# Kernel tuning notes

Hardware: AMD Instinct MI355X
Metric: run time of the kernel (lower is better)

## Reference

```python
import jax, jax.numpy as jnp
import numpy as np

B, N, E = 4, 2048, 512
H = 8
HD = E // H
HIDDEN = 3 * E  # split_ratio=3
EPS = 1e-5


def _layernorm(x, g, b):
    mu = jnp.mean(x, axis=-1, keepdims=True)
    var = jnp.var(x, axis=-1, keepdims=True)
    return (x - mu) * jax.lax.rsqrt(var + EPS) * g + b


def setup_inputs() -> dict:
    key = jax.random.key(0)
    ks = jax.random.split(key, 7)
    s = 0.02
    return {
        "x": jax.random.normal(ks[0], (B, N, E), jnp.float32),
        "qkv_w": jax.random.normal(ks[1], (E, 3 * E), jnp.float32) * s,
        "qkv_b": jax.random.normal(ks[2], (3 * E,), jnp.float32) * s,
        "fc1_w": jax.random.normal(ks[3], (E, HIDDEN), jnp.float32) * s,
        "fc1_b": jax.random.normal(ks[4], (HIDDEN,), jnp.float32) * s,
        "fc2_w": jax.random.normal(ks[5], (HIDDEN, E), jnp.float32) * s,
        "fc2_b": jax.random.normal(ks[6], (E,), jnp.float32) * s,
        "ln_att_g": jnp.ones((E,), jnp.float32),
        "ln_att_b": jnp.zeros((E,), jnp.float32),
        "ln_ffn_g": jnp.ones((E,), jnp.float32),
        "ln_ffn_b": jnp.zeros((E,), jnp.float32),
    }


def reference(x, qkv_w, qkv_b, fc1_w, fc1_b, fc2_w, fc2_b,
              ln_att_g, ln_att_b, ln_ffn_g, ln_ffn_b):
    # --- attention sub-block (pre-norm) ---
    h = x
    xn = _layernorm(x, ln_att_g, ln_att_b)
    qkv = xn @ qkv_w + qkv_b                     # [B,N,3E]
    qkv = qkv.reshape(B, N, H, 3 * HD).transpose(0, 2, 1, 3)  # [B,H,N,3*HD]
    q, k, v = jnp.split(qkv, 3, axis=-1)         # each [B,H,N,HD]
    scale = HD ** -0.5
    scores = jnp.einsum("bhnd,bhmd->bhnm", q, k) * scale
    attn = jax.nn.softmax(scores, axis=-1)
    out = jnp.einsum("bhnm,bhmd->bhnd", attn, v)
    out = out.transpose(0, 2, 1, 3).reshape(B, N, E)
    x = out + h
    # --- FFN sub-block (pre-norm) ---
    h = x
    xn = _layernorm(x, ln_ffn_g, ln_ffn_b)
    y = jax.nn.gelu(xn @ fc1_w + fc1_b, approximate=False)
    y = y @ fc2_w + fc2_b
    return y + h
```

## Files before the change

### kernel.cpp

```cpp
#include <hip/hip_runtime.h>
#include <hip/hip_bf16.h>
#include <math.h>

typedef unsigned short ushort_t;
typedef unsigned int   uint32;

typedef __bf16 bf16x8 __attribute__((ext_vector_type(8)));
typedef float  floatx4 __attribute__((ext_vector_type(4)));

__device__ __forceinline__ float lo16(uint32 u) { return __uint_as_float(u << 16); }
__device__ __forceinline__ float hi16(uint32 u) { return __uint_as_float(u & 0xFFFF0000u); }
__device__ __forceinline__ float b2f(ushort_t u) { return __uint_as_float(((uint32)u) << 16); }
__device__ __forceinline__ ushort_t f2b(float f) {
    uint32 x = __float_as_uint(f);
    x += 0x7FFFu + ((x >> 16) & 1u);
    return (ushort_t)(x >> 16);
}
__device__ __forceinline__ bool bf_mode(const uint32* sniff) {
    return *sniff == 0x3F803F80u;
}
__device__ __forceinline__ float rd(const void* p, size_t i, bool bf) {
    return bf ? b2f(((const ushort_t*)p)[i]) : ((const float*)p)[i];
}
__device__ __forceinline__ float4 rd4(const void* p, size_t i, bool bf) {
    if (bf) {
        uint2 u = *(const uint2*)((const ushort_t*)p + i);
        float4 r; r.x = lo16(u.x); r.y = hi16(u.x); r.z = lo16(u.y); r.w = hi16(u.y);
        return r;
    }
    return *(const float4*)((const float*)p + i);
}
__device__ __forceinline__ float fexp2(float x) {
#if __has_builtin(__builtin_amdgcn_exp2f)
    return __builtin_amdgcn_exp2f(x);
#else
    return exp2f(x);
#endif
}
__device__ __forceinline__ void async_cp16(const ushort_t* g, ushort_t* l) {
    __builtin_amdgcn_global_load_lds(
        (const __attribute__((address_space(1))) void*)g,
        (__attribute__((address_space(3))) void*)l, 16, 0, 0);
}
__device__ __forceinline__ float gelu_f(float x) {
    float u = 0.79788456f * x * (1.0f + 0.044715f * x * x);
    u = fminf(u, 40.0f);
    float e = exp2f(u * 2.88539008f);
    return x * e * __builtin_amdgcn_rcpf(e + 1.0f);
}

__global__ __launch_bounds__(256)
void sentinel(float* out, float val, int n)
{
    int i = blockIdx.x * 256 + threadIdx.x;
    if (i < n) out[i] = val;
}

__global__ __launch_bounds__(256)
void conv_transpose3(const void* __restrict__ w0, const void* __restrict__ w1,
                     const void* __restrict__ w2, ushort_t* __restrict__ t0,
                     ushort_t* __restrict__ t1, ushort_t* __restrict__ t2,
                     const uint32* __restrict__ sniff)
{
    __shared__ ushort_t s[32][33];
    bool bf = bf_mode(sniff);
    int z = blockIdx.y;
    const void* W  = (z == 0) ? w0 : (z == 1) ? w1 : w2;
    ushort_t* Wt   = (z == 0) ? t0 : (z == 1) ? t1 : t2;
    int K = (z == 2) ? 1536 : 512;
    int N = (z == 2) ? 512 : 1536;
    int nb = N >> 5;
    int bx = blockIdx.x;
    int n0 = (bx % nb) * 32, k0 = (bx / nb) * 32;

    int tx = threadIdx.x & 31, ty = threadIdx.x >> 5;
#pragma unroll
    for (int i = 0; i < 4; i++) {
        int r = ty + i * 8;
        size_t idx = (size_t)(k0 + r) * N + (n0 + tx);
        s[r][tx] = f2b(rd(W, idx, bf));
    }
    __syncthreads();
#pragma unroll
    for (int i = 0; i < 4; i++) {
        int r = ty + i * 8;
        Wt[(size_t)(n0 + r) * K + (k0 + tx)] = s[tx][r];
    }
}

__global__ __launch_bounds__(256)
void v_transpose(const ushort_t* __restrict__ hbuf, ushort_t* __restrict__ vt)
{
    __shared__ ushort_t s[32][33];
    int tx = threadIdx.x & 31, ty = threadIdx.x >> 5;
    int n0 = blockIdx.x * 32, d0 = blockIdx.y * 32;
    int bh = blockIdx.z;
    int b = bh >> 3, h = bh & 7;
#pragma unroll
    for (int i = 0; i < 4; i++) {
        int r = ty + i * 8;
        s[r][tx] = hbuf[(size_t)(b * 2048 + n0 + r) * 1536 + h * 192 + 128 + d0 + tx];
    }
    __syncthreads();
#pragma unroll
    for (int i = 0; i < 4; i++) {
        int r = ty + i * 8;
        vt[((size_t)bh * 64 + d0 + r) * 2048 + n0 + tx] = s[tx][r];
    }
}

template <int XMODE>
__global__ __launch_bounds__(256)
void ln_any(const void* __restrict__ x, const void* __restrict__ g,
            const void* __restrict__ bta, ushort_t* __restrict__ out,
            const uint32* __restrict__ sniff)
{
    bool bf = bf_mode(sniff);
    int wid = threadIdx.x >> 6, lane = threadIdx.x & 63;
    int row = blockIdx.x * 4 + wid;
    size_t base = (size_t)row * 512 + (size_t)lane * 8;

    float4 v0, v1;
    if (XMODE == 2) { v0 = rd4(x, base, false); v1 = rd4(x, base + 4, false); }
    else            { v0 = rd4(x, base, bf);    v1 = rd4(x, base + 4, bf); }
    float v[8] = {v0.x, v0.y, v0.z, v0.w, v1.x, v1.y, v1.z, v1.w};

    float s = 0.f, ss = 0.f;
#pragma unroll
    for (int i = 0; i < 8; i++) { s += v[i]; ss += v[i] * v[i]; }
#pragma unroll
    for (int off = 32; off; off >>= 1) {
        s  += __shfl_xor(s, off);
        ss += __shfl_xor(ss, off);
    }
    float mu  = s * (1.0f / 512.0f);
    float var = ss * (1.0f / 512.0f) - mu * mu;
    float rs  = rsqrtf(var + 1e-5f);

    float4 g0 = rd4(g, lane * 8, bf), g1 = rd4(g, lane * 8 + 4, bf);
    float4 b0 = rd4(bta, lane * 8, bf), b1 = rd4(bta, lane * 8 + 4, bf);
    float gv[8] = {g0.x, g0.y, g0.z, g0.w, g1.x, g1.y, g1.z, g1.w};
    float bv[8] = {b0.x, b0.y, b0.z, b0.w, b1.x, b1.y, b1.z, b1.w};

    ushort_t o[8];
#pragma unroll
    for (int i = 0; i < 8; i++) o[i] = f2b((v[i] - mu) * rs * gv[i] + bv[i]);
    uint4 ov;
    ov.x = (uint32)o[0] | ((uint32)o[1] << 16);
    ov.y = (uint32)o[2] | ((uint32)o[3] << 16);
    ov.z = (uint32)o[4] | ((uint32)o[5] << 16);
    ov.w = (uint32)o[6] | ((uint32)o[7] << 16);
    *(uint4*)(out + base) = ov;
}

template <int TJ, int MODE>
__global__ __launch_bounds__(256)
void gemm_bt(const ushort_t* __restrict__ A, const ushort_t* __restrict__ Bt,
             const void* __restrict__ bias, void* C,
             const float* resid, int M, int N, int K,
             const uint32* __restrict__ sniff)
{
    constexpr int BN = 32 * TJ;
    __shared__ ushort_t As[128][32];
    __shared__ ushort_t Bs[BN][32];

    bool bf = bf_mode(sniff);
    int tid = threadIdx.x;
    int wid = tid >> 6, lane = tid & 63;
    int m0 = blockIdx.y * 128, n0 = blockIdx.x * BN;
    int wm = (wid >> 1) * 64, wn = (wid & 1) * (16 * TJ);
    int lm = lane & 15, kq = lane >> 4;

    floatx4 acc[4][TJ];
#pragma unroll
    for (int i = 0; i < 4; i++)
#pragma unroll
        for (int j = 0; j < TJ; j++) acc[i][j] = (floatx4)(0.f);

    for (int k0 = 0; k0 < K; k0 += 32) {
        __syncthreads();
#pragma unroll
        for (int i = 0; i < 2; i++) {
            int lin = i * 256 + tid;
            int r = lin >> 2, c8 = (lin & 3) * 8;
            async_cp16(&A[(size_t)(m0 + r) * K + k0 + c8], &As[r][c8]);
        }
#pragma unroll
        for (int i = 0; i < BN / 64; i++) {
            int lin = i * 256 + tid;
            int r = lin >> 2, c8 = (lin & 3) * 8;
            async_cp16(&Bt[(size_t)(n0 + r) * K + k0 + c8], &Bs[r][c8]);
        }
        __syncthreads();

        bf16x8 af[4], bfr[TJ];
#pragma unroll
        for (int ti = 0; ti < 4; ti++)
            af[ti] = *(const bf16x8*)&As[wm + ti * 16 + lm][kq * 8];
#pragma unroll
        for (int tj = 0; tj < TJ; tj++)
            bfr[tj] = *(const bf16x8*)&Bs[wn + tj * 16 + lm][kq * 8];
#pragma unroll
        for (int ti = 0; ti < 4; ti++)
#pragma unroll
            for (int tj = 0; tj < TJ; tj++)
                acc[ti][tj] = __builtin_amdgcn_mfma_f32_16x16x32_bf16(
                    af[ti], bfr[tj], acc[ti][tj], 0, 0, 0);
    }

    float bv[TJ];
#pragma unroll
    for (int tj = 0; tj < TJ; tj++) bv[tj] = rd(bias, n0 + wn + tj * 16 + lm, bf);
#pragma unroll
    for (int ti = 0; ti < 4; ti++) {
        int grow_base = m0 + wm + ti * 16 + kq * 4;
#pragma unroll
        for (int tj = 0; tj < TJ; tj++) {
            int gcol = n0 + wn + tj * 16 + lm;
#pragma unroll
            for (int r = 0; r < 4; r++) {
                int grow = grow_base + r;
                float v = acc[ti][tj][r] + bv[tj];
                if (MODE == 1) v = gelu_f(v);
                if (MODE == 2) {
                    float rv = resid[(size_t)grow * N + gcol];
                    ((float*)C)[(size_t)grow * N + gcol] = v + rv;
                } else {
                    ((ushort_t*)C)[(size_t)grow * N + gcol] = f2b(v);
                }
            }
        }
    }
}

template <int MODE>
__global__ __launch_bounds__(256)
void vgemm(const ushort_t* __restrict__ A, const void* __restrict__ W,
           const void* __restrict__ bias, void* C,
           const float* resid, int M, int N, int K,
             const uint32* __restrict__ sniff)
{
    __shared__ float Ast[32][33];
    __shared__ float Bs[32][36];

    bool bf = bf_mode(sniff);
    int t  = threadIdx.x;
    int tx = t & 15, ty = t >> 4;
    int m0 = blockIdx.y * 32, n0 = blockIdx.x * 32;
    int sr = t >> 3, sc4 = (t & 7) * 4;

    float a00 = 0.f, a01 = 0.f, a10 = 0.f, a11 = 0.f;

    for (int k0 = 0; k0 < K; k0 += 32) {
        __syncthreads();
        {
            uint2 u = *(const uint2*)&A[(size_t)(m0 + sr) * K + k0 + sc4];
            Ast[sc4 + 0][sr] = lo16(u.x);
            Ast[sc4 + 1][sr] = hi16(u.x);
            Ast[sc4 + 2][sr] = lo16(u.y);
            Ast[sc4 + 3][sr] = hi16(u.y);
        }
        {
            float4 w = rd4(W, (size_t)(k0 + sr) * N + n0 + sc4, bf);
            *(float4*)&Bs[sr][sc4] = w;
        }
        __syncthreads();

#pragma unroll
        for (int kk = 0; kk < 32; kk++) {
            float av0 = Ast[kk][ty], av1 = Ast[kk][ty + 16];
            float bv0 = Bs[kk][tx],  bv1 = Bs[kk][tx + 16];
            a00 += av0 * bv0; a01 += av0 * bv1;
            a10 += av1 * bv0; a11 += av1 * bv1;
        }
    }

    float accs[4] = {a00, a01, a10, a11};
#pragma unroll
    for (int q = 0; q < 4; q++) {
        int row = m0 + ty + (q >> 1) * 16;
        int col = n0 + tx + (q & 1) * 16;
        float v = accs[q] + rd(bias, col, bf);
        if (MODE == 1) v = gelu_f(v);
        if (MODE == 2) {
            float rv = resid[(size_t)row * N + col];
            ((float*)C)[(size_t)row * N + col] = v + rv;
        } else {
            ((ushort_t*)C)[(size_t)row * N + col] = f2b(v);
        }
    }
}

__global__ __launch_bounds__(256)
void attn_flash(const ushort_t* __restrict__ qkv, const ushort_t* __restrict__ vt,
                const void* __restrict__ x, float* __restrict__ out,
                const uint32* __restrict__ sniff)
{
    __shared__ ushort_t Kl[64][72];
    __shared__ ushort_t Vl[64][72];
    __shared__ ushort_t Pl[128][68];

    bool bf = bf_mode(sniff);
    int tid = threadIdx.x;
    int wid = tid >> 6, lane = tid & 63;
    int lm = lane & 15, quad = lane >> 4;
    int qt = blockIdx.x & 15;
    int h  = (blockIdx.x >> 4) & 7;
    int b  = blockIdx.x >> 7;
    int bh = b * 8 + h;
    int q0 = qt * 128;

    const float SC = 0.18033688011f;

    bf16x8 qf[2][2];
#pragma unroll
    for (int g = 0; g < 2; g++) {
        const ushort_t* qp = qkv +
            ((size_t)(b * 2048 + q0 + wid * 32 + g * 16 + lm) * 1536 + h * 192);
        union { bf16x8 v; ushort_t u[8]; } qa0, qa1;
        qa0.v = *(const bf16x8*)(qp + quad * 8);
        qa1.v = *(const bf16x8*)(qp + 32 + quad * 8);
#pragma unroll
        for (int i = 0; i < 8; i++) {
            qa0.u[i] = f2b(b2f(qa0.u[i]) * SC);
            qa1.u[i] = f2b(b2f(qa1.u[i]) * SC);
        }
        qf[g][0] = qa0.v; qf[g][1] = qa1.v;
    }

    floatx4 oacc[2][4];
#pragma unroll
    for (int g = 0; g < 2; g++)
#pragma unroll
        for (int dt = 0; dt < 4; dt++) oacc[g][dt] = (floatx4)(0.f);
    float lsum[2][4];
#pragma unroll
    for (int g = 0; g < 2; g++)
#pragma unroll
        for (int r = 0; r < 4; r++) lsum[g][r] = 0.f;

    int srow = tid >> 3;
    int sc8  = (tid & 7) * 8;

    const ushort_t* kb0 = qkv + ((size_t)(b * 2048 + srow)      * 1536 + h * 192 + 64 + sc8);
    const ushort_t* kb1 = qkv + ((size_t)(b * 2048 + 32 + srow) * 1536 + h * 192 + 64 + sc8);
    const ushort_t* vb0 = vt + ((size_t)bh * 64 + srow)      * 2048 + sc8;
    const ushort_t* vb1 = vt + ((size_t)bh * 64 + 32 + srow) * 2048 + sc8;

    uint4 kr0 = *(const uint4*)(kb0);
    uint4 kr1 = *(const uint4*)(kb1);
    uint4 vr0 = *(const uint4*)(vb0);
    uint4 vr1 = *(const uint4*)(vb1);

    for (int kv = 0; kv < 2048; kv += 64) {
        __syncthreads();
        *(uint4*)&Kl[srow][sc8]      = kr0;
        *(uint4*)&Kl[32 + srow][sc8] = kr1;
        *(uint4*)&Vl[srow][sc8]      = vr0;
        *(uint4*)&Vl[32 + srow][sc8] = vr1;
        __syncthreads();

        {
            int nkv = (kv + 64) & 2047;
            kr0 = *(const uint4*)(kb0 + (size_t)nkv * 1536);
            kr1 = *(const uint4*)(kb1 + (size_t)nkv * 1536);
            vr0 = *(const uint4*)(vb0 + nkv);
            vr1 = *(const uint4*)(vb1 + nkv);
        }

        floatx4 sacc[2][4];
#pragma unroll
        for (int g = 0; g < 2; g++)
#pragma unroll
            for (int t = 0; t < 4; t++) sacc[g][t] = (floatx4)(0.f);
        __builtin_amdgcn_s_setprio(1);
#pragma unroll
        for (int t = 0; t < 4; t++) {
            bf16x8 kf0 = *(const bf16x8*)&Kl[t * 16 + lm][quad * 8];
            bf16x8 kf1 = *(const bf16x8*)&Kl[t * 16 + lm][32 + quad * 8];
#pragma unroll
            for (int g = 0; g < 2; g++) {
                sacc[g][t] = __builtin_amdgcn_mfma_f32_16x16x32_bf16(qf[g][0], kf0, sacc[g][t], 0, 0, 0);
                sacc[g][t] = __builtin_amdgcn_mfma_f32_16x16x32_bf16(qf[g][1], kf1, sacc[g][t], 0, 0, 0);
            }
        }
        __builtin_amdgcn_s_setprio(0);

#pragma unroll
        for (int g = 0; g < 2; g++)
#pragma unroll
            for (int t = 0; t < 4; t++) {
#pragma unroll
                for (int r = 0; r < 4; r++) {
                    float pv = fexp2(sacc[g][t][r]);
                    lsum[g][r] += pv;
                    Pl[wid * 32 + g * 16 + quad * 4 + r][t * 16 + lm] =
                        (ushort_t)(__float_as_uint(pv) >> 16);
                }
            }

        bf16x8 pf[2][2];
#pragma unroll
        for (int g = 0; g < 2; g++) {
            pf[g][0] = *(const bf16x8*)&Pl[wid * 32 + g * 16 + lm][quad * 8];
            pf[g][1] = *(const bf16x8*)&Pl[wid * 32 + g * 16 + lm][32 + quad * 8];
        }
        __builtin_amdgcn_s_setprio(1);
#pragma unroll
        for (int dt = 0; dt < 4; dt++) {
            bf16x8 vf0 = *(const bf16x8*)&Vl[dt * 16 + lm][quad * 8];
            bf16x8 vf1 = *(const bf16x8*)&Vl[dt * 16 + lm][32 + quad * 8];
#pragma unroll
            for (int g = 0; g < 2; g++) {
                oacc[g][dt] = __builtin_amdgcn_mfma_f32_16x16x32_bf16(pf[g][0], vf0, oacc[g][dt], 0, 0, 0);
                oacc[g][dt] = __builtin_amdgcn_mfma_f32_16x16x32_bf16(pf[g][1], vf1, oacc[g][dt], 0, 0, 0);
            }
        }
        __builtin_amdgcn_s_setprio(0);
    }

    float rinv[2][4];
#pragma unroll
    for (int g = 0; g < 2; g++)
#pragma unroll
        for (int r = 0; r < 4; r++) {
            float rs = lsum[g][r];
            rs += __shfl_xor(rs, 1);
            rs += __shfl_xor(rs, 2);
            rs += __shfl_xor(rs, 4);
            rs += __shfl_xor(rs, 8);
            rinv[g][r] = __builtin_amdgcn_rcpf(rs);
        }

#pragma unroll
    for (int g = 0; g < 2; g++)
#pragma unroll
        for (int dt = 0; dt < 4; dt++) {
#pragma unroll
            for (int r = 0; r < 4; r++) {
                int row = q0 + wid * 32 + g * 16 + quad * 4 + r;
                int col = h * 64 + dt * 16 + lm;
                size_t idx = (size_t)(b * 2048 + row) * 512 + col;
                out[idx] = oacc[g][dt][r] * rinv[g][r] + rd(x, idx, bf);
            }
        }
}

extern "C" void kernel_launch(void* const* d_in, const int* in_sizes, int n_in,
                              void* d_out, int out_size, void* d_ws, size_t ws_size,
                              hipStream_t stream)
{
    static const int expect[11] = {4194304, 786432, 1536, 786432, 1536, 786432,
                                   512, 512, 512, 512, 512};
    bool ok = (n_in == 11);
    if (ok) for (int i = 0; i < 11; i++) if (in_sizes[i] != expect[i]) { ok = false; break; }
    int nblk = (out_size + 255) / 256;
    if (!ok) {
        sentinel<<<nblk, 256, 0, stream>>>((float*)d_out, 1.0e6f, out_size);
        return;
    }
    if (ws_size < (size_t)33554432) {
        sentinel<<<nblk, 256, 0, stream>>>((float*)d_out, 2.0e6f, out_size);
        return;
    }

    const void* x     = d_in[0];
    const void* qkv_w = d_in[1];
    const void* qkv_b = d_in[2];
    const void* fc1_w = d_in[3];
    const void* fc1_b = d_in[4];
    const void* fc2_w = d_in[5];
    const void* fc2_b = d_in[6];
    const void* ln1g  = d_in[7];
    const void* ln1b  = d_in[8];
    const void* ln2g  = d_in[9];
    const void* ln2b  = d_in[10];
    const uint32* sniff = (const uint32*)d_in[7];

    char* ws = (char*)d_ws;
    ushort_t* xn   = (ushort_t*)(ws);
    ushort_t* hbuf = (ushort_t*)(ws + 8388608);
    float*    x2   = (float*)d_out;
    ushort_t* vt   = xn;

    bool mfma_path = (ws_size >= (size_t)38273024);

    if (mfma_path) {
        ushort_t* wtq = (ushort_t*)(ws + 33554432);
        ushort_t* wt1 = (ushort_t*)(ws + 35127296);
        ushort_t* wt2 = (ushort_t*)(ws + 36700160);

        conv_transpose3<<<dim3(768, 3), 256, 0, stream>>>(qkv_w, fc1_w, fc2_w,
                                                          wtq, wt1, wt2, sniff);
        ln_any<0><<<2048, 256, 0, stream>>>(x, ln1g, ln1b, xn, sniff);
        gemm_bt<4, 0><<<dim3(12, 64), 256, 0, stream>>>(xn, wtq, qkv_b, hbuf, nullptr,
                                                        8192, 1536, 512, sniff);
        v_transpose<<<dim3(64, 2, 32), 256, 0, stream>>>(hbuf, vt);
        attn_flash<<<512, 256, 0, stream>>>(hbuf, vt, x, x2, sniff);
        ln_any<2><<<2048, 256, 0, stream>>>(x2, ln2g, ln2b, xn, sniff);
        gemm_bt<4, 1><<<dim3(12, 64), 256, 0, stream>>>(xn, wt1, fc1_b, hbuf, nullptr,
                                                        8192, 1536, 512, sniff);
        gemm_bt<2, 2><<<dim3(8, 64), 256, 0, stream>>>(hbuf, wt2, fc2_b, d_out, x2,
                                                       8192, 512, 1536, sniff);
    } else {
        ln_any<0><<<2048, 256, 0, stream>>>(x, ln1g, ln1b, xn, sniff);
        vgemm<0><<<dim3(48, 256), 256, 0, stream>>>(xn, qkv_w, qkv_b, hbuf, nullptr,
                                                    8192, 1536, 512, sniff);
        v_transpose<<<dim3(64, 2, 32), 256, 0, stream>>>(hbuf, vt);
        attn_flash<<<512, 256, 0, stream>>>(hbuf, vt, x, x2, sniff);
        ln_any<2><<<2048, 256, 0, stream>>>(x2, ln2g, ln2b, xn, sniff);
        vgemm<1><<<dim3(48, 256), 256, 0, stream>>>(xn, fc1_w, fc1_b, hbuf, nullptr,
                                                    8192, 1536, 512, sniff);
        vgemm<2><<<dim3(16, 256), 256, 0, stream>>>(hbuf, fc2_w, fc2_b, d_out, x2,
                                                    8192, 512, 1536, sniff);
    }
}
```

Measured before the change: 265.8 us.

## Double-buffer flash attention K/V, keep P in registers via bpermute, swizzle blocks

The attention kernel now double-buffers K/V tiles in LDS, which removes one barrier per iteration. It computes S transposed (K as the A operand) so each lane holds one query column, and it packs the probabilities into bf16 and redistributes them with ds_bpermute, removing the LDS round trip through the Pl buffer. Row sums are reduced across quads instead of within 16 lanes. Block IDs in both the GEMM and attention kernels are remapped in groups of eight to improve cache locality, at the cost of extra permute instructions and more LDS for the second buffer.

```diff
diff --git a/kernel.cpp b/kernel.cpp
--- a/kernel.cpp
+++ b/kernel.cpp
@@ -35,6 +35,13 @@
     return __builtin_amdgcn_exp2f(x);
 #else
     return exp2f(x);
+#endif
+}
+__device__ __forceinline__ uint32 pack_bf16(float e0, float e1) {
+#if __has_builtin(__builtin_amdgcn_perm)
+    return __builtin_amdgcn_perm(__float_as_uint(e1), __float_as_uint(e0), 0x07060302u);
+#else
+    return (__float_as_uint(e0) >> 16) | (__float_as_uint(e1) & 0xFFFF0000u);
 #endif
 }
 __device__ __forceinline__ void async_cp16(const ushort_t* g, ushort_t* l) {
@@ -167,7 +174,13 @@
     bool bf = bf_mode(sniff);
     int tid = threadIdx.x;
     int wid = tid >> 6, lane = tid & 63;
-    int m0 = blockIdx.y * 128, n0 = blockIdx.x * BN;
+
+    int nwgx = gridDim.x;
+    int wg   = blockIdx.y * nwgx + blockIdx.x;
+    int cpx  = (nwgx * gridDim.y) >> 3;
+    int swz  = (wg & 7) * cpx + (wg >> 3);
+    int m0 = (swz / nwgx) * 128, n0 = (swz % nwgx) * BN;
+
     int wm = (wid >> 1) * 64, wn = (wid & 1) * (16 * TJ);
     int lm = lane & 15, kq = lane >> 4;
 
@@ -296,17 +309,19 @@
                 const void* __restrict__ x, float* __restrict__ out,
                 const uint32* __restrict__ sniff)
 {
-    __shared__ ushort_t Kl[64][72];
-    __shared__ ushort_t Vl[64][72];
-    __shared__ ushort_t Pl[128][68];
+    __shared__ ushort_t Kl[2][64][72];
+    __shared__ ushort_t Vl[2][64][72];
 
     bool bf = bf_mode(sniff);
     int tid = threadIdx.x;
     int wid = tid >> 6, lane = tid & 63;
     int lm = lane & 15, quad = lane >> 4;
-    int qt = blockIdx.x & 15;
-    int h  = (blockIdx.x >> 4) & 7;
-    int b  = blockIdx.x >> 7;
+
+    int bid = blockIdx.x;
+    int swz = (bid & 7) * 64 + (bid >> 3);
+    int qt = swz & 15;
+    int h  = (swz >> 4) & 7;
+    int b  = swz >> 7;
     int bh = b * 8 + h;
     int q0 = qt * 128;
 
@@ -333,11 +348,7 @@
     for (int g = 0; g < 2; g++)
 #pragma unroll
         for (int dt = 0; dt < 4; dt++) oacc[g][dt] = (floatx4)(0.f);
-    float lsum[2][4];
-#pragma unroll
-    for (int g = 0; g < 2; g++)
-#pragma unroll
-        for (int r = 0; r < 4; r++) lsum[g][r] = 0.f;
+    float lsum[2] = {0.f, 0.f};
 
     int srow = tid >> 3;
     int sc8  = (tid & 7) * 8;
@@ -351,17 +362,28 @@
     uint4 kr1 = *(const uint4*)(kb1);
     uint4 vr0 = *(const uint4*)(vb0);
     uint4 vr1 = *(const uint4*)(vb1);
-
+    *(uint4*)&Kl[0][srow][sc8]      = kr0;
+    *(uint4*)&Kl[0][32 + srow][sc8] = kr1;
+    *(uint4*)&Vl[0][srow][sc8]      = vr0;
+    *(uint4*)&Vl[0][32 + srow][sc8] = vr1;
+    kr0 = *(const uint4*)(kb0 + (size_t)64 * 1536);
+    kr1 = *(const uint4*)(kb1 + (size_t)64 * 1536);
+    vr0 = *(const uint4*)(vb0 + 64);
+    vr1 = *(const uint4*)(vb1 + 64);
+    __syncthreads();
+
+    int addr0 = (lm + ((quad & 1) << 5)) << 2;
+    int addr1 = addr0 + 64;
+    bool hiq  = (quad >> 1) != 0;
+
+    int p = 0;
     for (int kv = 0; kv < 2048; kv += 64) {
-        __syncthreads();
-        *(uint4*)&Kl[srow][sc8]      = kr0;
-        *(uint4*)&Kl[32 + srow][sc8] = kr1;
-        *(uint4*)&Vl[srow][sc8]      = vr0;
-        *(uint4*)&Vl[32 + srow][sc8] = vr1;
-        __syncthreads();
-
-        {
-            int nkv = (kv + 64) & 2047;
+        if (kv < 2048 - 64) {
+            *(uint4*)&Kl[p ^ 1][srow][sc8]      = kr0;
+            *(uint4*)&Kl[p ^ 1][32 + srow][sc8] = kr1;
+            *(uint4*)&Vl[p ^ 1][srow][sc8]      = vr0;
+            *(uint4*)&Vl[p ^ 1][32 + srow][sc8] = vr1;
+            int nkv = (kv + 128) & 2047;
             kr0 = *(const uint4*)(kb0 + (size_t)nkv * 1536);
             kr1 = *(const uint4*)(kb1 + (size_t)nkv * 1536);
             vr0 = *(const uint4*)(vb0 + nkv);
@@ -376,40 +398,55 @@
         __builtin_amdgcn_s_setprio(1);
 #pragma unroll
         for (int t = 0; t < 4; t++) {
-            bf16x8 kf0 = *(const bf16x8*)&Kl[t * 16 + lm][quad * 8];
-            bf16x8 kf1 = *(const bf16x8*)&Kl[t * 16 + lm][32 + quad * 8];
+            bf16x8 kf0 = *(const bf16x8*)&Kl[p][t * 16 + lm][quad * 8];
+            bf16x8 kf1 = *(const bf16x8*)&Kl[p][t * 16 + lm][32 + quad * 8];
 #pragma unroll
             for (int g = 0; g < 2; g++) {
-                sacc[g][t] = __builtin_amdgcn_mfma_f32_16x16x32_bf16(qf[g][0], kf0, sacc[g][t], 0, 0, 0);
-                sacc[g][t] = __builtin_amdgcn_mfma_f32_16x16x32_bf16(qf[g][1], kf1, sacc[g][t], 0, 0, 0);
+                sacc[g][t] = __builtin_amdgcn_mfma_f32_16x16x32_bf16(kf0, qf[g][0], sacc[g][t], 0, 0, 0);
+                sacc[g][t] = __builtin_amdgcn_mfma_f32_16x16x32_bf16(kf1, qf[g][1], sacc[g][t], 0, 0, 0);
             }
         }
         __builtin_amdgcn_s_setprio(0);
 
-#pragma unroll
-        for (int g = 0; g < 2; g++)
+        uint32 pk[2][4][2];
+#pragma unroll
+        for (int g = 0; g < 2; g++) {
 #pragma unroll
             for (int t = 0; t < 4; t++) {
-#pragma unroll
-                for (int r = 0; r < 4; r++) {
-                    float pv = fexp2(sacc[g][t][r]);
-                    lsum[g][r] += pv;
-                    Pl[wid * 32 + g * 16 + quad * 4 + r][t * 16 + lm] =
-                        (ushort_t)(__float_as_uint(pv) >> 16);
+                float e0 = fexp2(sacc[g][t][0]);
+                float e1 = fexp2(sacc[g][t][1]);
+                float e2 = fexp2(sacc[g][t][2]);
+                float e3 = fexp2(sacc[g][t][3]);
+                lsum[g] += (e0 + e1) + (e2 + e3);
+                pk[g][t][0] = pack_bf16(e0, e1);
+                pk[g][t][1] = pack_bf16(e2, e3);
+            }
+        }
+
+        bf16x8 pf[2][2];
+#pragma unroll
+        for (int g = 0; g < 2; g++) {
+#pragma unroll
+            for (int c = 0; c < 2; c++) {
+                uint32 pw[4];
+#pragma unroll
+                for (int j = 0; j < 4; j++) {
+                    int ad = (j >> 1) ? addr1 : addr0;
+                    int va = __builtin_amdgcn_ds_bpermute(ad, (int)pk[g][2 * c][j & 1]);
+                    int vb = __builtin_amdgcn_ds_bpermute(ad, (int)pk[g][2 * c + 1][j & 1]);
+                    pw[j] = (uint32)(hiq ? vb : va);
                 }
+                union { uint4 u; bf16x8 v; } cv;
+                cv.u = make_uint4(pw[0], pw[1], pw[2], pw[3]);
+                pf[g][c] = cv.v;
             }
-
-        bf16x8 pf[2][2];
-#pragma unroll
-        for (int g = 0; g < 2; g++) {
-            pf[g][0] = *(const bf16x8*)&Pl[wid * 32 + g * 16 + lm][quad * 8];
-            pf[g][1] = *(const bf16x8*)&Pl[wid * 32 + g * 16 + lm][32 + quad * 8];
-        }
+        }
+
         __builtin_amdgcn_s_setprio(1);
 #pragma unroll
         for (int dt = 0; dt < 4; dt++) {
-            bf16x8 vf0 = *(const bf16x8*)&Vl[dt * 16 + lm][quad * 8];
-            bf16x8 vf1 = *(const bf16x8*)&Vl[dt * 16 + lm][32 + quad * 8];
+            bf16x8 vf0 = *(const bf16x8*)&Vl[p][dt * 16 + lm][quad * 8];
+            bf16x8 vf1 = *(const bf16x8*)&Vl[p][dt * 16 + lm][32 + quad * 8];
 #pragma unroll
             for (int g = 0; g < 2; g++) {
                 oacc[g][dt] = __builtin_amdgcn_mfma_f32_16x16x32_bf16(pf[g][0], vf0, oacc[g][dt], 0, 0, 0);
@@ -417,20 +454,22 @@
             }
         }
         __builtin_amdgcn_s_setprio(0);
+
+        __syncthreads();
+        p ^= 1;
     }
 
     float rinv[2][4];
 #pragma unroll
-    for (int g = 0; g < 2; g++)
-#pragma unroll
-        for (int r = 0; r < 4; r++) {
-            float rs = lsum[g][r];
-            rs += __shfl_xor(rs, 1);
-            rs += __shfl_xor(rs, 2);
-            rs += __shfl_xor(rs, 4);
-            rs += __shfl_xor(rs, 8);
-            rinv[g][r] = __builtin_amdgcn_rcpf(rs);
-        }
+    for (int g = 0; g < 2; g++) {
+        float rs = lsum[g];
+        rs += __shfl_xor(rs, 16);
+        rs += __shfl_xor(rs, 32);
+        float ri = __builtin_amdgcn_rcpf(rs);
+#pragma unroll
+        for (int r = 0; r < 4; r++)
+            rinv[g][r] = __shfl(ri, quad * 4 + r);
+    }
 
 #pragma unroll
     for (int g = 0; g < 2; g++)
```

Result: no change. 260.6 us (-2.0%).
